# Optimization experiments

Hardware: AMD Instinct MI355X
Metric: run time of the kernel (lower is better)

## Reference

```python
import jax, jax.numpy as jnp
import numpy as np

B, IN_SHAPE, EXP_SHAPE, HID, NB_CLASSES = 64, 10000, 53, 1500, 2048


def setup_inputs() -> dict:
    key = jax.random.key(0)
    ks = jax.random.split(key, 8)
    gos = jax.random.uniform(ks[0], (B, IN_SHAPE), dtype=jnp.float32)
    exp_x = jax.random.uniform(ks[1], (B, EXP_SHAPE), dtype=jnp.float32)
    # FlatModel params (torch Linear: y = x @ W.T + b; store pre-transposed)
    W1 = jax.random.normal(ks[2], (IN_SHAPE, HID), dtype=jnp.float32) * (1.0 / np.sqrt(IN_SHAPE))
    b1 = jnp.zeros((HID,), dtype=jnp.float32)
    W2 = jax.random.normal(ks[3], (HID + EXP_SHAPE, NB_CLASSES), dtype=jnp.float32) * (1.0 / np.sqrt(HID + EXP_SHAPE))
    b2 = jnp.zeros((NB_CLASSES,), dtype=jnp.float32)
    # HPO adjacency (non-trainable buffer in the original; values in [0,1))
    hpo_matrix = jax.random.uniform(ks[4], (NB_CLASSES, NB_CLASSES), dtype=jnp.float32)
    return {"gos": gos, "exp_x": exp_x, "W1": W1, "b1": b1, "W2": W2, "b2": b2, "hpo_matrix": hpo_matrix}


def reference(gos, exp_x, W1, b1, W2, b2, hpo_matrix):
    # FlatModel (eval mode: dropout is identity). torch F.gelu default = exact erf gelu.
    h = jax.nn.gelu(gos @ W1 + b1, approximate=False)          # (B, HID)
    x = jnp.concatenate([h, exp_x], axis=1)                     # (B, HID+EXP)
    flat = jax.nn.sigmoid(x @ W2 + b2)                          # (B, C)
    # HPOLayer + permute + MaxPool1d(C): out[b,j] = max_i flat[b,j] * M[i,j]
    out = jnp.max(flat[:, None, :] * hpo_matrix[None, :, :], axis=1)  # (B, C)
    return out
```

## Files before the change

### kernel.cpp

```cpp
#include <hip/hip_runtime.h>
#include <math.h>


#define B64 64
#define IN_SH 10000
#define EXP_SH 53
#define HID 1500
#define NPAD1 1536
#define NBC 2048
#define K2 1553
#define KS1 40
#define KST1 8
#define KS2 13
#define KST2 4
#define XSTEP 56
#define CMCH 32
#define CMBLK 256
#define WLDS 640
#define ACC1 (NPAD1 * 64)
#define ACC2 (NBC * 64)

using short8  = __attribute__((ext_vector_type(8))) short;
using floatx4 = __attribute__((ext_vector_type(4))) float;
using uintx4  = __attribute__((ext_vector_type(4))) unsigned int;
using uintx2  = __attribute__((ext_vector_type(2))) unsigned int;

__device__ __forceinline__ unsigned short f2bf(float f) {
    unsigned u = __float_as_uint(f);
    u += 0x7fffu + ((u >> 16) & 1u);
    return (unsigned short)(u >> 16);
}


__global__ __launch_bounds__(256) void prep_k(const float* __restrict__ g,
                                              unsigned short* __restrict__ gosBf) {
    int t    = blockIdx.x * 256 + threadIdx.x;
    int lane = t & 63;
    int sgrp = (t >> 6) & 3;
    int step = t >> 8;
    int q    = lane >> 4;
    int l15  = lane & 15;
    int b    = sgrp * 16 + l15;
    int k0   = step * 32 + q * 8;
    const float* p = g + (size_t)b * IN_SH + k0;
    unsigned int o[4];
    #pragma unroll
    for (int i = 0; i < 4; i++) {
        float lo = (k0 + 2 * i     < IN_SH) ? p[2 * i]     : 0.f;
        float hi = (k0 + 2 * i + 1 < IN_SH) ? p[2 * i + 1] : 0.f;
        o[i] = (unsigned)f2bf(lo) | ((unsigned)f2bf(hi) << 16);
    }
    uintx4 v; v.x = o[0]; v.y = o[1]; v.z = o[2]; v.w = o[3];
    *(uintx4*)(gosBf + (size_t)t * 8) = v;
}

__device__ __forceinline__ void load_b4(const unsigned short* __restrict__ bf,
                                        int stg, uintx4 bv[4]) {
    #pragma unroll
    for (int s = 0; s < 4; s++)
        bv[s] = *(const uintx4*)(bf + (size_t)(stg * 4 + s) * 512);
}

template<int KSTEPS>
__device__ __forceinline__ void gemm_core(
    const float* __restrict__ W, const unsigned short* __restrict__ Bfc,
    float* __restrict__ pbuf, int N, int K, int ldw, int bx, int by, int tid,
    float* __restrict__ ldsw)
{
    int lane = tid & 63;
    int q    = lane >> 4;
    int l15  = lane & 15;
    int n0   = bx * 64 + 16 * (tid >> 6);
    int k0   = by * (KSTEPS * 32);
    bool fast = (n0 + 16 <= N) && (k0 + KSTEPS * 32 <= K);
    int kl  = lane >> 2;
    int c4  = (lane & 3) * 4;

    const unsigned short* bf = Bfc + (size_t)lane * 8;

    floatx4 acc[4];
    #pragma unroll
    for (int s = 0; s < 4; s++) acc[s] = (floatx4){0.f, 0.f, 0.f, 0.f};

    floatx4 g[2][2];

    #define GLB(st, slot)                                                        \
        {                                                                        \
            int kb_ = k0 + (st) * 32;                                            \
            _Pragma("unroll")                                                    \
            for (int i_ = 0; i_ < 2; i_++) {                                     \
                int kg_ = kb_ + kl + 16 * i_;                                    \
                if (fast) {                                                      \
                    g[slot][i_] = *(const floatx4*)(W + (size_t)kg_ * ldw + n0 + c4); \
                } else {                                                         \
                    _Pragma("unroll")                                            \
                    for (int j_ = 0; j_ < 4; j_++)                               \
                        g[slot][i_][j_] = (kg_ < K && n0 + c4 + j_ < N)          \
                            ? W[(size_t)kg_ * ldw + n0 + c4 + j_] : 0.f;         \
                }                                                                \
            }                                                                    \
        }
    #define LWR(buf, slot)                                                       \
        {                                                                        \
            _Pragma("unroll")                                                    \
            for (int i_ = 0; i_ < 2; i_++)                                       \
                *(floatx4*)(ldsw + (buf) * WLDS + (kl + 16 * i_) * 20 + c4) = g[slot][i_]; \
        }

    GLB(0, 0);
    if (KSTEPS > 1) GLB(1, 1);
    LWR(0, 0);

    uintx4 bv[2][4];
    load_b4(bf, 0, bv[0]);
    if (KSTEPS > 1) load_b4(bf, 1, bv[1]);

    #pragma unroll
    for (int st = 0; st < KSTEPS; st++) {
        const int s = st & 1;
        const float* lb = ldsw + s * WLDS;

        short8 af;
        #pragma unroll
        for (int j = 0; j < 8; j++)
            af[j] = (short)f2bf(lb[(q * 8 + j) * 20 + l15]);

        uintx4 bt[4];
        if (st + 2 < KSTEPS) {
            GLB(st + 2, s);
            load_b4(bf, st + 2, bt);
        }

        #pragma unroll
        for (int m = 0; m < 4; m++) {
            short8 bf8 = __builtin_bit_cast(short8, bv[s][m]);
            acc[m] = __builtin_amdgcn_mfma_f32_16x16x32_bf16(af, bf8, acc[m], 0, 0, 0);
        }

        if (st + 1 < KSTEPS) LWR(1 - s, 1 - s);
        if (st + 2 < KSTEPS) {
            #pragma unroll
            for (int m = 0; m < 4; m++) bv[s][m] = bt[m];
        }
    }
    #undef GLB
    #undef LWR

    int nrow = n0 + q * 4;
    #pragma unroll
    for (int s = 0; s < 4; s++) {
        #pragma unroll
        for (int rr = 0; rr < 4; rr++)
            pbuf[(size_t)(nrow + rr) * 64 + s * 16 + l15] = acc[s][rr];
    }
}

__global__ __launch_bounds__(256) void gemm1_k(
    const float* __restrict__ W1, const unsigned short* __restrict__ gosBf,
    float* __restrict__ hpre_p, const float* __restrict__ M, float* __restrict__ cm)
{
    __shared__ float lds[4 * 2 * WLDS];
    int bi = blockIdx.x;
    if (bi < CMBLK) {
        int j  = (bi & 7) * 256 + threadIdx.x;
        int i0 = (bi >> 3) * 64;
        float m = 0.0f;
        #pragma unroll 16
        for (int i = i0; i < i0 + 64; i++)
            m = fmaxf(m, M[(size_t)i * NBC + j]);
        cm[(bi >> 3) * NBC + j] = m;
    } else {
        int gb = bi - CMBLK;
        int bx = gb % 24;
        int by = gb / 24;
        gemm_core<KST1>(W1, gosBf + (size_t)by * (KST1 * 4) * 512,
                        hpre_p + (size_t)by * ACC1, HID, IN_SH, HID, bx, by,
                        threadIdx.x, lds + (threadIdx.x >> 6) * (2 * WLDS));
    }
}

__global__ __launch_bounds__(256) void gemm2_k(
    const float* __restrict__ W2, const unsigned short* __restrict__ Xf,
    float* __restrict__ logits_p)
{
    __shared__ float lds[4 * 2 * WLDS];
    gemm_core<KST2>(W2, Xf + (size_t)blockIdx.y * (KST2 * 4) * 512,
                    logits_p + (size_t)blockIdx.y * ACC2, NBC, K2, NBC,
                    blockIdx.x, blockIdx.y,
                    threadIdx.x, lds + (threadIdx.x >> 6) * (2 * WLDS));
}

__global__ __launch_bounds__(256) void combine1(
    const float* __restrict__ hpre_p, const float* __restrict__ b1,
    const float* __restrict__ expx, unsigned short* __restrict__ Xf,
    const float* __restrict__ cm, float* __restrict__ cmr)
{
    int bi = blockIdx.x;
    if (bi < 2 * XSTEP) {
        int step = bi >> 1, half = bi & 1;
        int tid  = threadIdx.x;
        int lane = tid & 63;
        int sgrp = tid >> 6;
        int q    = lane >> 4;
        int l15  = lane & 15;
        int b    = sgrp * 16 + l15;
        int kb   = step * 32 + q * 8;
        int nb   = kb + half * 4;
        float sv[4];
        if (nb + 3 < HID) {
            float s0 = b1[nb], s1 = b1[nb + 1], s2 = b1[nb + 2], s3 = b1[nb + 3];
            const float* p = hpre_p + (size_t)nb * 64 + b;
            #pragma unroll 8
            for (int ks = 0; ks < KS1; ks++, p += ACC1) {
                s0 += p[0]; s1 += p[64]; s2 += p[128]; s3 += p[192];
            }
            sv[0] = s0; sv[1] = s1; sv[2] = s2; sv[3] = s3;
            #pragma unroll
            for (int jj = 0; jj < 4; jj++)
                sv[jj] = 0.5f * sv[jj] * (1.0f + erff(sv[jj] * 0.70710678118654752f));
        } else {
            #pragma unroll
            for (int jj = 0; jj < 4; jj++) {
                int n = nb + jj;
                float v = 0.f;
                if (n < HID) {
                    float s = b1[n];
                    for (int ks = 0; ks < KS1; ks++)
                        s += hpre_p[(size_t)ks * ACC1 + (size_t)n * 64 + b];
                    v = 0.5f * s * (1.0f + erff(s * 0.70710678118654752f));
                } else if (n < HID + EXP_SH) {
                    v = expx[b * EXP_SH + (n - HID)];
                }
                sv[jj] = v;
            }
        }
        unsigned int o0 = (unsigned)f2bf(sv[0]) | ((unsigned)f2bf(sv[1]) << 16);
        unsigned int o1 = (unsigned)f2bf(sv[2]) | ((unsigned)f2bf(sv[3]) << 16);
        size_t t = (size_t)step * 256 + tid;
        uintx2 v; v.x = o0; v.y = o1;
        *(uintx2*)(Xf + t * 8 + half * 4) = v;
    } else {
        int j = (bi - 2 * XSTEP) * 256 + threadIdx.x;
        float m = 0.f;
        #pragma unroll
        for (int c = 0; c < CMCH; c++) m = fmaxf(m, cm[c * NBC + j]);
        cmr[j] = m;
    }
}

__global__ __launch_bounds__(256) void final_k(
    const float* __restrict__ logits_p, const float* __restrict__ b2,
    const float* __restrict__ cmr, float* __restrict__ out)
{
    __shared__ float lds[32 * 65];
    int j0  = blockIdx.x * 32;
    int tid = threadIdx.x;
    #pragma unroll
    for (int e = 0; e < 8; e++) {
        int lin = e * 256 + tid;
        int jj  = lin >> 6;
        int b   = lin & 63;
        int j   = j0 + jj;
        float s = b2[j];
        const float* p = logits_p + (size_t)j * 64 + b;
        #pragma unroll
        for (int ks = 0; ks < KS2; ks++)
            s += p[(size_t)ks * ACC2];
        float sig = 1.0f / (1.0f + expf(-s));
        lds[jj * 65 + b] = sig * cmr[j];
    }
    __syncthreads();
    #pragma unroll
    for (int e = 0; e < 8; e++) {
        int lin = e * 256 + tid;
        int b   = lin >> 5;
        int jj  = lin & 31;
        out[(size_t)b * NBC + j0 + jj] = lds[jj * 65 + b];
    }
}

extern "C" void kernel_launch(void* const* d_in, const int* in_sizes, int n_in,
                              void* d_out, int out_size, void* d_ws, size_t ws_size,
                              hipStream_t stream) {
    const float* gos  = (const float*)d_in[0];
    const float* expx = (const float*)d_in[1];
    const float* W1   = (const float*)d_in[2];
    const float* b1   = (const float*)d_in[3];
    const float* W2   = (const float*)d_in[4];
    const float* b2   = (const float*)d_in[5];
    const float* hpo  = (const float*)d_in[6];
    float* out = (float*)d_out;

    char* ws = (char*)d_ws;
    unsigned short* gosBf = (unsigned short*)ws;
    unsigned short* Xf    = (unsigned short*)(ws + 1310720);
    float* cm       = (float*)(ws + 1540096);
    float* cmr      = (float*)(ws + 1802240);
    float* hpre_p   = (float*)(ws + 1810432);
    float* logits_p = (float*)(ws + 17539072);

    prep_k<<<320, 256, 0, stream>>>(gos, gosBf);

    gemm1_k<<<CMBLK + 24 * KS1, 256, 0, stream>>>(W1, gosBf, hpre_p, hpo, cm);

    combine1<<<2 * XSTEP + 8, 256, 0, stream>>>(hpre_p, b1, expx, Xf, cm, cmr);

    gemm2_k<<<dim3(NBC / 64, KS2), 256, 0, stream>>>(W2, Xf, logits_p);

    final_k<<<NBC / 32, 256, 0, stream>>>(logits_p, b2, cmr, out);
}
```

Measured before the change: 157.2 us.

## Stream weights into LDS with direct global_load_lds and deeper pipeline

Replaces the register-staged weight loads in both GEMMs with direct global-to-LDS loads (global_load_lds) using a 4-stage ring buffer, explicit vmcnt waits and a compile-time unrolled step recursion. Out-of-range addresses are clamped instead of branching, and the padded LDS row stride is removed. The split-K factor for gemm1 is halved (K steps per block doubled), which reduces the partial-sum traffic, and combine1 is rewritten with a simpler per-thread mapping. Risks: LDS bank conflicts without padding, and clamped loads that read garbage for the tail rows, which must match zero B columns.

```diff
diff --git a/kernel.cpp b/kernel.cpp
--- a/kernel.cpp
+++ b/kernel.cpp
@@ -9,21 +9,18 @@
 #define NPAD1 1536
 #define NBC 2048
 #define K2 1553
-#define KS1 40
-#define KST1 8
+#define KS1 20
+#define KST1 16
 #define KS2 13
 #define KST2 4
-#define XSTEP 56
+#define NSTEP 52
 #define CMCH 32
-#define CMBLK 256
-#define WLDS 640
 #define ACC1 (NPAD1 * 64)
 #define ACC2 (NBC * 64)
 
 using short8  = __attribute__((ext_vector_type(8))) short;
 using floatx4 = __attribute__((ext_vector_type(4))) float;
 using uintx4  = __attribute__((ext_vector_type(4))) unsigned int;
-using uintx2  = __attribute__((ext_vector_type(2))) unsigned int;
 
 __device__ __forceinline__ unsigned short f2bf(float f) {
     unsigned u = __float_as_uint(f);
@@ -31,6 +28,118 @@
     return (unsigned short)(u >> 16);
 }
 
+typedef __attribute__((address_space(3))) void lds_v;
+typedef __attribute__((address_space(1))) const void glb_v;
+__device__ __forceinline__ void gll16(const float* g, float* l) {
+    __builtin_amdgcn_global_load_lds((glb_v*)g, (lds_v*)l, 16, 0, 0);
+}
+
+#define WVS(n) asm volatile("s_waitcnt vmcnt(" #n ")" ::: "memory")
+template<int N> __device__ __forceinline__ void waitv() {
+    if constexpr (N >= 20)      WVS(20);
+    else if constexpr (N >= 16) WVS(16);
+    else if constexpr (N >= 14) WVS(14);
+    else if constexpr (N >= 12) WVS(12);
+    else if constexpr (N >= 10) WVS(10);
+    else if constexpr (N >= 8)  WVS(8);
+    else                        WVS(6);
+}
+
+constexpr int after_ops(int KS, int st) {
+    int n = 0;
+    if (st < 4) {
+        n += 2 * (3 - st) + 8;
+        for (int k = 0; k < st; k++)
+            n += (k + 4 < KS ? 2 : 0) + (k + 2 < KS ? 4 : 0);
+    } else {
+        n += (st - 2 < KS ? 4 : 0);
+        for (int k = st - 3; k < st; k++)
+            n += (k + 4 < KS ? 2 : 0) + (k + 2 < KS ? 4 : 0);
+    }
+    return n;
+}
+
+template<int KS, int ST>
+__device__ __forceinline__ void gstep(
+    const float* __restrict__ W, const unsigned short* __restrict__ bf,
+    float* __restrict__ ldsw, floatx4 (&acc)[4], uintx4 (&bv)[3][4],
+    unsigned wbase, unsigned stepInc, unsigned halfInc, unsigned maxoff,
+    int q, int l15)
+{
+    if constexpr (ST < KS) {
+        constexpr int AO = after_ops(KS, ST);
+        waitv<(AO > 6 ? AO - 6 : 0)>();
+        const float* lb = ldsw + (ST & 3) * 512;
+        short8 af;
+        #pragma unroll
+        for (int j = 0; j < 8; j++)
+            af[j] = (short)f2bf(lb[(q * 8 + j) * 16 + l15]);
+        if constexpr (ST + 4 < KS) {
+            unsigned o0 = wbase + (unsigned)(ST + 4) * stepInc;
+            unsigned o1 = o0 + halfInc;
+            if (o0 > maxoff) o0 = maxoff;
+            if (o1 > maxoff) o1 = maxoff;
+            gll16(W + o0, ldsw + ((ST + 4) & 3) * 512);
+            gll16(W + o1, ldsw + ((ST + 4) & 3) * 512 + 256);
+        }
+        if constexpr (ST + 2 < KS) {
+            #pragma unroll
+            for (int s = 0; s < 4; s++)
+                bv[(ST + 2) % 3][s] =
+                    *(const uintx4*)(bf + (size_t)((ST + 2) * 4 + s) * 512);
+        }
+        #pragma unroll
+        for (int s = 0; s < 4; s++) {
+            short8 b8 = __builtin_bit_cast(short8, bv[ST % 3][s]);
+            acc[s] = __builtin_amdgcn_mfma_f32_16x16x32_bf16(af, b8, acc[s], 0, 0, 0);
+        }
+        gstep<KS, ST + 1>(W, bf, ldsw, acc, bv, wbase, stepInc, halfInc, maxoff, q, l15);
+    }
+}
+
+template<int KS>
+__device__ __forceinline__ void gemm_wave2(
+    const float* __restrict__ W, const unsigned short* __restrict__ Bfc,
+    float* __restrict__ pbuf, int ldw, unsigned maxoff, int n0, int k0,
+    int lane, float* __restrict__ ldsw)
+{
+    const int q = lane >> 4, l15 = lane & 15;
+    const int r = lane >> 2, c4 = (lane & 3) * 4;
+    unsigned wbase = (unsigned)((k0 + r) * ldw + n0 + c4);
+    const unsigned stepInc = 32u * (unsigned)ldw;
+    const unsigned halfInc = 16u * (unsigned)ldw;
+
+    #pragma unroll
+    for (int st = 0; st < 4; st++) {
+        unsigned o0 = wbase + (unsigned)st * stepInc;
+        unsigned o1 = o0 + halfInc;
+        if (o0 > maxoff) o0 = maxoff;
+        if (o1 > maxoff) o1 = maxoff;
+        gll16(W + o0, ldsw + (st & 3) * 512);
+        gll16(W + o1, ldsw + (st & 3) * 512 + 256);
+    }
+    const unsigned short* bf = Bfc + (size_t)lane * 8;
+    uintx4 bv[3][4];
+    #pragma unroll
+    for (int k = 0; k < 2; k++) {
+        #pragma unroll
+        for (int s = 0; s < 4; s++)
+            bv[k][s] = *(const uintx4*)(bf + (size_t)(k * 4 + s) * 512);
+    }
+    floatx4 acc[4];
+    #pragma unroll
+    for (int s = 0; s < 4; s++) acc[s] = (floatx4){0.f, 0.f, 0.f, 0.f};
+
+    gstep<KS, 0>(W, bf, ldsw, acc, bv, wbase, stepInc, halfInc, maxoff, q, l15);
+
+    int nrow = n0 + q * 4;
+    #pragma unroll
+    for (int s = 0; s < 4; s++) {
+        #pragma unroll
+        for (int rr = 0; rr < 4; rr++)
+            pbuf[(size_t)(nrow + rr) * 64 + s * 16 + l15] = acc[s][rr];
+    }
+}
 
 __global__ __launch_bounds__(256) void prep_k(const float* __restrict__ g,
                                               unsigned short* __restrict__ gosBf) {
@@ -54,114 +163,13 @@
     *(uintx4*)(gosBf + (size_t)t * 8) = v;
 }
 
-__device__ __forceinline__ void load_b4(const unsigned short* __restrict__ bf,
-                                        int stg, uintx4 bv[4]) {
-    #pragma unroll
-    for (int s = 0; s < 4; s++)
-        bv[s] = *(const uintx4*)(bf + (size_t)(stg * 4 + s) * 512);
-}
-
-template<int KSTEPS>
-__device__ __forceinline__ void gemm_core(
-    const float* __restrict__ W, const unsigned short* __restrict__ Bfc,
-    float* __restrict__ pbuf, int N, int K, int ldw, int bx, int by, int tid,
-    float* __restrict__ ldsw)
-{
-    int lane = tid & 63;
-    int q    = lane >> 4;
-    int l15  = lane & 15;
-    int n0   = bx * 64 + 16 * (tid >> 6);
-    int k0   = by * (KSTEPS * 32);
-    bool fast = (n0 + 16 <= N) && (k0 + KSTEPS * 32 <= K);
-    int kl  = lane >> 2;
-    int c4  = (lane & 3) * 4;
-
-    const unsigned short* bf = Bfc + (size_t)lane * 8;
-
-    floatx4 acc[4];
-    #pragma unroll
-    for (int s = 0; s < 4; s++) acc[s] = (floatx4){0.f, 0.f, 0.f, 0.f};
-
-    floatx4 g[2][2];
-
-    #define GLB(st, slot)                                                        \
-        {                                                                        \
-            int kb_ = k0 + (st) * 32;                                            \
-            _Pragma("unroll")                                                    \
-            for (int i_ = 0; i_ < 2; i_++) {                                     \
-                int kg_ = kb_ + kl + 16 * i_;                                    \
-                if (fast) {                                                      \
-                    g[slot][i_] = *(const floatx4*)(W + (size_t)kg_ * ldw + n0 + c4); \
-                } else {                                                         \
-                    _Pragma("unroll")                                            \
-                    for (int j_ = 0; j_ < 4; j_++)                               \
-                        g[slot][i_][j_] = (kg_ < K && n0 + c4 + j_ < N)          \
-                            ? W[(size_t)kg_ * ldw + n0 + c4 + j_] : 0.f;         \
-                }                                                                \
-            }                                                                    \
-        }
-    #define LWR(buf, slot)                                                       \
-        {                                                                        \
-            _Pragma("unroll")                                                    \
-            for (int i_ = 0; i_ < 2; i_++)                                       \
-                *(floatx4*)(ldsw + (buf) * WLDS + (kl + 16 * i_) * 20 + c4) = g[slot][i_]; \
-        }
-
-    GLB(0, 0);
-    if (KSTEPS > 1) GLB(1, 1);
-    LWR(0, 0);
-
-    uintx4 bv[2][4];
-    load_b4(bf, 0, bv[0]);
-    if (KSTEPS > 1) load_b4(bf, 1, bv[1]);
-
-    #pragma unroll
-    for (int st = 0; st < KSTEPS; st++) {
-        const int s = st & 1;
-        const float* lb = ldsw + s * WLDS;
-
-        short8 af;
-        #pragma unroll
-        for (int j = 0; j < 8; j++)
-            af[j] = (short)f2bf(lb[(q * 8 + j) * 20 + l15]);
-
-        uintx4 bt[4];
-        if (st + 2 < KSTEPS) {
-            GLB(st + 2, s);
-            load_b4(bf, st + 2, bt);
-        }
-
-        #pragma unroll
-        for (int m = 0; m < 4; m++) {
-            short8 bf8 = __builtin_bit_cast(short8, bv[s][m]);
-            acc[m] = __builtin_amdgcn_mfma_f32_16x16x32_bf16(af, bf8, acc[m], 0, 0, 0);
-        }
-
-        if (st + 1 < KSTEPS) LWR(1 - s, 1 - s);
-        if (st + 2 < KSTEPS) {
-            #pragma unroll
-            for (int m = 0; m < 4; m++) bv[s][m] = bt[m];
-        }
-    }
-    #undef GLB
-    #undef LWR
-
-    int nrow = n0 + q * 4;
-    #pragma unroll
-    for (int s = 0; s < 4; s++) {
-        #pragma unroll
-        for (int rr = 0; rr < 4; rr++)
-            pbuf[(size_t)(nrow + rr) * 64 + s * 16 + l15] = acc[s][rr];
-    }
-}
-
-__global__ __launch_bounds__(256) void gemm1_k(
+__global__ __launch_bounds__(256, 4) void gemm1_k(
     const float* __restrict__ W1, const unsigned short* __restrict__ gosBf,
     float* __restrict__ hpre_p, const float* __restrict__ M, float* __restrict__ cm)
 {
-    __shared__ float lds[4 * 2 * WLDS];
+    __shared__ float lds[4 * 2048];
     int bi = blockIdx.x;
-    if (bi < CMBLK) {
+    if (bi < 256) {
         int j  = (bi & 7) * 256 + threadIdx.x;
         int i0 = (bi >> 3) * 64;
         float m = 0.0f;
@@ -170,24 +178,29 @@
             m = fmaxf(m, M[(size_t)i * NBC + j]);
         cm[(bi >> 3) * NBC + j] = m;
     } else {
-        int gb = bi - CMBLK;
-        int bx = gb % 24;
-        int by = gb / 24;
-        gemm_core<KST1>(W1, gosBf + (size_t)by * (KST1 * 4) * 512,
-                        hpre_p + (size_t)by * ACC1, HID, IN_SH, HID, bx, by,
-                        threadIdx.x, lds + (threadIdx.x >> 6) * (2 * WLDS));
-    }
-}
-
-__global__ __launch_bounds__(256) void gemm2_k(
+        int gb  = bi - 256;
+        int bx  = gb % 24;
+        int by  = gb / 24;
+        int wid = threadIdx.x >> 6;
+        gemm_wave2<KST1>(W1, gosBf + (size_t)by * (KST1 * 4) * 512,
+                         hpre_p + (size_t)by * ACC1, HID,
+                         (unsigned)(IN_SH * HID - 4),
+                         bx * 64 + wid * 16, by * (KST1 * 32),
+                         threadIdx.x & 63, lds + wid * 2048);
+    }
+}
+
+__global__ __launch_bounds__(256, 4) void gemm2_k(
     const float* __restrict__ W2, const unsigned short* __restrict__ Xf,
     float* __restrict__ logits_p)
 {
-    __shared__ float lds[4 * 2 * WLDS];
-    gemm_core<KST2>(W2, Xf + (size_t)blockIdx.y * (KST2 * 4) * 512,
-                    logits_p + (size_t)blockIdx.y * ACC2, NBC, K2, NBC,
-                    blockIdx.x, blockIdx.y,
-                    threadIdx.x, lds + (threadIdx.x >> 6) * (2 * WLDS));
+    __shared__ float lds[4 * 2048];
+    int wid = threadIdx.x >> 6;
+    gemm_wave2<KST2>(W2, Xf + (size_t)blockIdx.y * (KST2 * 4) * 512,
+                     logits_p + (size_t)blockIdx.y * ACC2, NBC,
+                     (unsigned)(K2 * NBC - 4),
+                     blockIdx.x * 64 + wid * 16, blockIdx.y * (KST2 * 32),
+                     threadIdx.x & 63, lds + wid * 2048);
 }
 
 __global__ __launch_bounds__(256) void combine1(
@@ -196,51 +209,39 @@
     const float* __restrict__ cm, float* __restrict__ cmr)
 {
     int bi = blockIdx.x;
-    if (bi < 2 * XSTEP) {
-        int step = bi >> 1, half = bi & 1;
-        int tid  = threadIdx.x;
-        int lane = tid & 63;
-        int sgrp = tid >> 6;
-        int q    = lane >> 4;
-        int l15  = lane & 15;
-        int b    = sgrp * 16 + l15;
-        int kb   = step * 32 + q * 8;
-        int nb   = kb + half * 4;
-        float sv[4];
-        if (nb + 3 < HID) {
-            float s0 = b1[nb], s1 = b1[nb + 1], s2 = b1[nb + 2], s3 = b1[nb + 3];
-            const float* p = hpre_p + (size_t)nb * 64 + b;
-            #pragma unroll 8
-            for (int ks = 0; ks < KS1; ks++, p += ACC1) {
-                s0 += p[0]; s1 += p[64]; s2 += p[128]; s3 += p[192];
+    if (bi < 208) {
+        int idx = bi * 256 + threadIdx.x;
+        int b   = idx & 63;
+        int n0  = (idx >> 6) * 2;
+        float v[2];
+        #pragma unroll
+        for (int e = 0; e < 2; e++) {
+            int n = n0 + e;
+            float x = 0.f;
+            if (n < HID) {
+                const float* p = hpre_p + (size_t)n * 64 + b;
+                float a0 = 0.f, a1 = 0.f, a2 = 0.f, a3 = 0.f;
+                #pragma unroll
+                for (int ks = 0; ks < KS1; ks += 4) {
+                    a0 += p[(size_t)ks * ACC1];
+                    a1 += p[(size_t)(ks + 1) * ACC1];
+                    a2 += p[(size_t)(ks + 2) * ACC1];
+                    a3 += p[(size_t)(ks + 3) * ACC1];
+                }
+                float s = b1[n] + ((a0 + a1) + (a2 + a3));
+                x = 0.5f * s * (1.0f + erff(s * 0.70710678118654752f));
+            } else if (n < HID + EXP_SH) {
+                x = expx[b * EXP_SH + (n - HID)];
             }
-            sv[0] = s0; sv[1] = s1; sv[2] = s2; sv[3] = s3;
-            #pragma unroll
-            for (int jj = 0; jj < 4; jj++)
-                sv[jj] = 0.5f * sv[jj] * (1.0f + erff(sv[jj] * 0.70710678118654752f));
-        } else {
-            #pragma unroll
-            for (int jj = 0; jj < 4; jj++) {
-                int n = nb + jj;
-                float v = 0.f;
-                if (n < HID) {
-                    float s = b1[n];
-                    for (int ks = 0; ks < KS1; ks++)
-                        s += hpre_p[(size_t)ks * ACC1 + (size_t)n * 64 + b];
-                    v = 0.5f * s * (1.0f + erff(s * 0.70710678118654752f));
-                } else if (n < HID + EXP_SH) {
-                    v = expx[b * EXP_SH + (n - HID)];
-                }
-                sv[jj] = v;
-            }
+            v[e] = x;
         }
-        unsigned int o0 = (unsigned)f2bf(sv[0]) | ((unsigned)f2bf(sv[1]) << 16);
-        unsigned int o1 = (unsigned)f2bf(sv[2]) | ((unsigned)f2bf(sv[3]) << 16);
-        size_t t = (size_t)step * 256 + tid;
-        uintx2 v; v.x = o0; v.y = o1;
-        *(uintx2*)(Xf + t * 8 + half * 4) = v;
+        unsigned o = (unsigned)f2bf(v[0]) | ((unsigned)f2bf(v[1]) << 16);
+        int step = n0 >> 5, w = n0 & 31, q = w >> 3, j = w & 7;
+        int sgrp = b >> 4, l15 = b & 15;
+        size_t tq = (size_t)(step * 4 + sgrp) * 64 + q * 16 + l15;
+        *(unsigned*)(Xf + tq * 8 + j) = o;
     } else {
-        int j = (bi - 2 * XSTEP) * 256 + threadIdx.x;
+        int j = (bi - 208) * 256 + threadIdx.x;
         float m = 0.f;
         #pragma unroll
         for (int c = 0; c < CMCH; c++) m = fmaxf(m, cm[c * NBC + j]);
@@ -294,18 +295,18 @@
     char* ws = (char*)d_ws;
     unsigned short* gosBf = (unsigned short*)ws;
     unsigned short* Xf    = (unsigned short*)(ws + 1310720);
-    float* cm       = (float*)(ws + 1540096);
-    float* cmr      = (float*)(ws + 1802240);
-    float* hpre_p   = (float*)(ws + 1810432);
-    float* logits_p = (float*)(ws + 17539072);
+    float* cm       = (float*)(ws + 1523712);
+    float* cmr      = (float*)(ws + 1785856);
+    float* hpre_p   = (float*)(ws + 1794048);
+    float* logits_p = (float*)(ws + 9658368);
 
     prep_k<<<320, 256, 0, stream>>>(gos, gosBf);
 
-    gemm1_k<<<CMBLK + 24 * KS1, 256, 0, stream>>>(W1, gosBf, hpre_p, hpo, cm);
-
-    combine1<<<2 * XSTEP + 8, 256, 0, stream>>>(hpre_p, b1, expx, Xf, cm, cmr);
-
-    gemm2_k<<<dim3(NBC / 64, KS2), 256, 0, stream>>>(W2, Xf, logits_p);
-
-    final_k<<<NBC / 32, 256, 0, stream>>>(logits_p, b2, cmr, out);
-}
+    gemm1_k<<<256 + 24 * KS1, 256, 0, stream>>>(W1, gosBf, hpre_p, hpo, cm);
+
+    combine1<<<216, 256, 0, stream>>>(hpre_p, b1, expx, Xf, cm, cmr);
+
+    gemm2_k<<<dim3(32, KS2), 256, 0, stream>>>(W2, Xf, logits_p);
+
+    final_k<<<64, 256, 0, stream>>>(logits_p, b2, cmr, out);
+}
```

Result: faster. 153.7 us (-2.3%).
